# Kernel optimization log

Measured on AMD Instinct MI355X. Metric: run time of the kernel, lower is better.

## Reference

```python
import jax, jax.numpy as jnp
import numpy as np

N, E, D, EDGE_DIM = 50000, 150000, 100, 200

def _w(key, fi, fo):
    return jax.random.normal(key, (fi, fo), dtype=jnp.float32) / np.float32(np.sqrt(fi))

def setup_inputs():
    key = jax.random.key(0)
    ks = jax.random.split(key, 40)
    inp = {}
    inp["x"] = jax.random.normal(ks[0], (N, D), dtype=jnp.float32)
    inp["msg"] = jax.random.normal(ks[1], (E, D), dtype=jnp.float32)
    # TimeEncoder: Linear(1, D)
    inp["time_w"] = _w(ks[2], 1, D)
    inp["time_b"] = jnp.zeros((D,), jnp.float32)
    # TransformerConv 1: in=100, heads=8, out=100, concat -> 800
    H1 = 8 * D
    inp["c1_qw"] = _w(ks[3], D, H1); inp["c1_qb"] = jnp.zeros((H1,), jnp.float32)
    inp["c1_kw"] = _w(ks[4], D, H1); inp["c1_kb"] = jnp.zeros((H1,), jnp.float32)
    inp["c1_vw"] = _w(ks[5], D, H1); inp["c1_vb"] = jnp.zeros((H1,), jnp.float32)
    inp["c1_ew"] = _w(ks[6], EDGE_DIM, H1)  # lin_edge has no bias in PyG
    inp["c1_sw"] = _w(ks[7], D, H1); inp["c1_sb"] = jnp.zeros((H1,), jnp.float32)
    # TransformerConv 2: in=800, heads=1, out=100, concat=False
    inp["c2_qw"] = _w(ks[8], H1, D); inp["c2_qb"] = jnp.zeros((D,), jnp.float32)
    inp["c2_kw"] = _w(ks[9], H1, D); inp["c2_kb"] = jnp.zeros((D,), jnp.float32)
    inp["c2_vw"] = _w(ks[10], H1, D); inp["c2_vb"] = jnp.zeros((D,), jnp.float32)
    inp["c2_ew"] = _w(ks[11], EDGE_DIM, D)
    inp["c2_sw"] = _w(ks[12], H1, D); inp["c2_sb"] = jnp.zeros((D,), jnp.float32)
    # LinkPredictor (in_channels=100, out=2)
    inp["lp_src_w"] = _w(ks[13], D, 2 * D); inp["lp_src_b"] = jnp.zeros((2 * D,), jnp.float32)
    inp["lp_dst_w"] = _w(ks[14], D, 2 * D); inp["lp_dst_b"] = jnp.zeros((2 * D,), jnp.float32)
    inp["lp1_w"] = _w(ks[15], 4 * D, 8 * D); inp["lp1_b"] = jnp.zeros((8 * D,), jnp.float32)
    inp["lp2_w"] = _w(ks[16], 8 * D, 2 * D); inp["lp2_b"] = jnp.zeros((2 * D,), jnp.float32)
    inp["lp3_w"] = _w(ks[17], 2 * D, D // 2); inp["lp3_b"] = jnp.zeros((D // 2,), jnp.float32)
    inp["lp4_w"] = _w(ks[18], D // 2, 2); inp["lp4_b"] = jnp.zeros((2,), jnp.float32)
    inp["last_update"] = jax.random.randint(ks[19], (N,), 0, 1000000)
    inp["t"] = jax.random.randint(ks[20], (E,), 0, 1000000)
    inp["edge_index"] = jax.random.randint(ks[21], (2, E), 0, N)
    return inp

def _tconv(x, src, dst, edge_attr, qw, qb, kw, kb, vw, vb, ew, sw, sb, heads, out_ch, concat, n):
    q = (x @ qw + qb).reshape(n, heads, out_ch)
    k = (x @ kw + kb).reshape(n, heads, out_ch)
    v = (x @ vw + vb).reshape(n, heads, out_ch)
    e = (edge_attr @ ew).reshape(-1, heads, out_ch)        # [E,H,C]
    kj = k[src] + e                                        # gather src keys + edge
    alpha = jnp.sum(q[dst] * kj, axis=-1) / np.float32(np.sqrt(out_ch))  # [E,H]
    amax = jax.ops.segment_max(alpha, dst, num_segments=n)
    ex = jnp.exp(alpha - amax[dst])
    denom = jax.ops.segment_sum(ex, dst, num_segments=n)
    a = ex / (denom[dst] + 1e-16)                          # per-dest softmax
    agg = jax.ops.segment_sum((v[src] + e) * a[..., None], dst, num_segments=n)
    out = agg.reshape(n, heads * out_ch) if concat else jnp.mean(agg, axis=1)
    return out + x @ sw + sb                               # root/skip connection

def reference(x, msg, time_w, time_b,
              c1_qw, c1_qb, c1_kw, c1_kb, c1_vw, c1_vb, c1_ew, c1_sw, c1_sb,
              c2_qw, c2_qb, c2_kw, c2_kb, c2_vw, c2_vb, c2_ew, c2_sw, c2_sb,
              lp_src_w, lp_src_b, lp_dst_w, lp_dst_b,
              lp1_w, lp1_b, lp2_w, lp2_b, lp3_w, lp3_b, lp4_w, lp4_b,
              last_update, t, edge_index):
    src, dst = edge_index[0], edge_index[1]
    rel_t = (last_update[src] - t).astype(jnp.float32)[:, None]  # [E,1]
    rel_enc = jnp.cos(rel_t @ time_w + time_b)                   # [E,D]
    edge_attr = jnp.concatenate([rel_enc, msg], axis=-1)         # [E,200]
    h = jax.nn.relu(_tconv(x, src, dst, edge_attr, c1_qw, c1_qb, c1_kw, c1_kb,
                           c1_vw, c1_vb, c1_ew, c1_sw, c1_sb, 8, D, True, N))
    h = jax.nn.relu(_tconv(h, src, dst, edge_attr, c2_qw, c2_qb, c2_kw, c2_kb,
                           c2_vw, c2_vb, c2_ew, c2_sw, c2_sb, 1, D, False, N))
    hh = jnp.concatenate([h[src] @ lp_src_w + lp_src_b,
                          h[dst] @ lp_dst_w + lp_dst_b], axis=-1)
    hh = jnp.tanh(hh @ lp1_w + lp1_b)
    hh = jnp.tanh(hh @ lp2_w + lp2_b)
    hh = jnp.tanh(hh @ lp3_w + lp3_b)
    return hh @ lp4_w + lp4_b
```

## Files before the change

### kernel.cpp

```cpp
#include <hip/hip_runtime.h>
#include <hip/hip_bf16.h>
#include <math.h>

typedef __hip_bfloat16 bf16;
typedef short s16x8 __attribute__((ext_vector_type(8)));
typedef float f32x4 __attribute__((ext_vector_type(4)));

#define NN 50000
#define EE 150000
#define EH 75000

static __device__ __forceinline__ float b2f(bf16 x){ return __bfloat162float(x); }
static __device__ __forceinline__ bf16 f2b(float x){ return __float2bfloat16(x); }
static __device__ __forceinline__ short f2s(float x){
  union { bf16 b; short s; } u; u.b = f2b(x); return u.s;
}
static __device__ __forceinline__ float u2f_lo(unsigned u){ union{unsigned i;float f;}c; c.i=u<<16; return c.f; }
static __device__ __forceinline__ float u2f_hi(unsigned u){ union{unsigned i;float f;}c; c.i=u&0xffff0000u; return c.f; }

static __device__ __forceinline__ float fast_tanh(float x){
  float a = fabsf(x);
  float e = __expf(2.0f*a);
  float t = 1.0f - __fdividef(2.0f, e + 1.0f);
  return x < 0.f ? -t : t;
}

static __device__ __forceinline__ void gload_lds16(const void* g, void* l){
  __builtin_amdgcn_global_load_lds((const __attribute__((address_space(1))) void*)g,
                                   (__attribute__((address_space(3))) void*)l, 16, 0, 0);
}

__global__ void k_zero(int* __restrict__ p, int n){
  int i = blockIdx.x*blockDim.x + threadIdx.x;
  if(i<n) p[i]=0;
}

__global__ void k_hist(const int* __restrict__ dst, int* __restrict__ deg){
  int i = blockIdx.x*blockDim.x + threadIdx.x;
  if(i<EE) atomicAdd(&deg[dst[i]], 1);
}

__global__ void k_scan(const int* __restrict__ deg, int* __restrict__ rowptr){
  __shared__ int part[1024];
  int tid = threadIdx.x;
  const int n = NN;
  int chunk = (n + 1023)/1024;
  int start = tid*chunk;
  int end = start + chunk; if(end > n) end = n;
  int s = 0;
  for(int i=start;i<end;i++) s += deg[i];
  part[tid] = s; __syncthreads();
  for(int off=1; off<1024; off<<=1){
    int v = (tid>=off)? part[tid-off] : 0;
    __syncthreads();
    part[tid] += v;
    __syncthreads();
  }
  int run = (tid==0)? 0 : part[tid-1];
  for(int i=start;i<end;i++){ rowptr[i]=run; run += deg[i]; }
  if(tid==0) rowptr[n] = part[1023];
}

__global__ void k_scatter(const int* __restrict__ dst, const int* __restrict__ rowptr,
                          int* __restrict__ cursor, int* __restrict__ elist){
  int e = blockIdx.x*blockDim.x + threadIdx.x;
  if(e<EE){ int d=dst[e]; int p=atomicAdd(&cursor[d],1); elist[rowptr[d]+p]=e; }
}

__global__ void k_relenc(const int* __restrict__ src, const int* __restrict__ tt,
                         const int* __restrict__ lu, const float* __restrict__ tw,
                         const float* __restrict__ tb, bf16* __restrict__ rel){
  int i = blockIdx.x*blockDim.x + threadIdx.x;
  if(i >= EE*112) return;
  int e = i/112, c = i - e*112;
  float v = 0.f;
  if(c < 100){
    float rt  = (float)(lu[src[e]] - tt[e]);
    float arg = __fadd_rn(__fmul_rn(rt, tw[c]), tb[c]);
    v = cosf(arg);
  }
  rel[i] = f2b(v);
}

__global__ void k_cvtpad(const float* __restrict__ in, int incols,
                         bf16* __restrict__ outp, int outcols, int total){
  int i = blockIdx.x*blockDim.x + threadIdx.x;
  if(i >= total) return;
  int r = i/outcols, c = i - r*outcols;
  outp[i] = f2b(c < incols ? in[(size_t)r*incols + c] : 0.f);
}

__global__ void k_wt2(const float* __restrict__ W, int K, int N, int colofs, int ncols,
                      bf16* __restrict__ WT, int kpad, int nrows){
  int i = blockIdx.x*blockDim.x + threadIdx.x;
  if(i >= nrows*kpad) return;
  int n = i / kpad, k = i - n*kpad;
  float v = (n<ncols && k<K)? W[(size_t)k*N + colofs + n] : 0.f;
  WT[i] = f2b(v);
}

__global__ void k_wtc1(const float* __restrict__ qw, const float* __restrict__ kw,
                       const float* __restrict__ vw, const float* __restrict__ sw,
                       bf16* __restrict__ outp){
  int i = blockIdx.x*blockDim.x + threadIdx.x;
  if(i >= 8*448*128) return;
  int h = i/(448*128), r = (i/128)%448, k = i&127;
  float v = 0.f;
  if(r < 400 && k < 100){
    int s = r/100, n = r - s*100;
    const float* W = s==0? qw : s==1? kw : s==2? vw : sw;
    v = W[(size_t)k*800 + h*100 + n];
  }
  outp[i] = f2b(v);
}

__global__ void k_wte(const float* __restrict__ ew, int N, int colofs,
                      bf16* __restrict__ outp){
  int i = blockIdx.x*blockDim.x + threadIdx.x;
  if(i >= 112*256) return;
  int r = i>>8, k = i&255;
  float v = 0.f;
  if(r < 100){
    if(k < 100) v = ew[(size_t)k*N + colofs + r];
    else if(k >= 128 && k < 228) v = ew[(size_t)(k-28)*N + colofs + r];
  }
  outp[i] = f2b(v);
}

__global__ void k_bstack(const float* __restrict__ b0, const float* __restrict__ b1,
                         const float* __restrict__ b2, const float* __restrict__ b3,
                         int W, int H, float* __restrict__ outp){
  int i = blockIdx.x*blockDim.x + threadIdx.x;
  if(i >= H*4*W) return;
  int h = i/(4*W), r = i - h*4*W, s = r/W, c = r - s*W;
  const float* b = s==0? b0 : s==1? b1 : s==2? b2 : b3;
  outp[i] = b[h*W + c];
}

template<int NT>
__global__ __launch_bounds__(256) void mm_tile(
    const bf16* __restrict__ A1, int lda1, int ksplit, int k1valid,
    const float* __restrict__ A2f, int lda2, int k2valid,
    const int* __restrict__ gather,
    const bf16* __restrict__ WT, int kpad,
    const bf16* __restrict__ zbuf,
    const float* __restrict__ bias,
    bf16* __restrict__ C, int ldc,
    int M, int nvalid, int act)
{
  constexpr int BN = NT*16;
  constexpr int BP = (BN*4 + 255)/256;
  constexpr int ABYTES = 128*32*2;
  constexpr int BBYTES = BN*32*2;
  constexpr int BUFSZ  = ABYTES + BBYTES;
  __shared__ __align__(16) char lds[2*BUFSZ];

  const int tid  = threadIdx.x;
  const int wave = tid>>6, lane = tid&63;
  const int quad = lane>>4, lo = lane&15;
  const int nstrip = blockIdx.y;
  WT += (size_t)nstrip*BN*kpad;
  C  += (size_t)nstrip*BN;
  if(bias) bias += nstrip*BN;
  const int nval = nvalid - nstrip*BN;
  const int row0 = blockIdx.x*128;

  const char*  a1base[2];
  const float* a2base[2];
  int acol0[2];
#pragma unroll
  for(int p=0;p<2;p++){
    int s = p*256 + tid;
    int row = s>>2, cp = s&3;
    int q = cp ^ ((row>>1)&3);
    int col0 = q*8;
    int rg = row0 + row; if(rg > M-1) rg = M-1;
    int ar = gather ? gather[rg] : rg;
    acol0[p]  = col0;
    a1base[p] = (const char*)A1 + ((size_t)ar*lda1 + col0)*2;
    a2base[p] = A2f ? (A2f + (size_t)ar*lda2 + col0 - ksplit) : nullptr;
  }
  const char* bbase[BP];
  bool bval[BP];
#pragma unroll
  for(int q=0;q<BP;q++){
    int s = q*256 + tid;
    int rb = s>>2, cp = s&3;
    int rbc = rb < BN ? rb : BN-1;
    int lq = cp ^ ((rbc>>1)&3);
    bval[q]  = (s < BN*4);
    bbase[q] = (const char*)WT + ((size_t)rbc*kpad + lq*8)*2;
  }

  f32x4 acc[2][NT];
#pragma unroll
  for(int m=0;m<2;m++)
#pragma unroll
    for(int n=0;n<NT;n++) acc[m][n] = (f32x4){0.f,0.f,0.f,0.f};

  float4 pf0[2], pf1[2];

  auto stageA1 = [&](char* buf, int kb){
#pragma unroll
    for(int p=0;p<2;p++){
      const char* s = (kb + acol0[p] < k1valid) ? (a1base[p] + (size_t)kb*2)
                                                : (const char*)zbuf;
      gload_lds16(s, buf + p*4096 + wave*1024);
    }
  };
  auto loadA2 = [&](int kb){
#pragma unroll
    for(int p=0;p<2;p++){
      int kk = kb - ksplit + acol0[p];
      const float* ap = a2base[p] + kb;
      pf0[p] = (kk   < k2valid) ? *(const float4*)ap     : (float4){0.f,0.f,0.f,0.f};
      pf1[p] = (kk+4 < k2valid) ? *(const float4*)(ap+4) : (float4){0.f,0.f,0.f,0.f};
    }
  };
  auto writeA2 = [&](char* buf){
#pragma unroll
    for(int p=0;p<2;p++){
      s16x8 v;
      v[0]=f2s(pf0[p].x); v[1]=f2s(pf0[p].y); v[2]=f2s(pf0[p].z); v[3]=f2s(pf0[p].w);
      v[4]=f2s(pf1[p].x); v[5]=f2s(pf1[p].y); v[6]=f2s(pf1[p].z); v[7]=f2s(pf1[p].w);
      *(s16x8*)(buf + p*4096 + (size_t)tid*16) = v;
    }
  };
  auto stageB = [&](char* buf, int kb){
#pragma unroll
    for(int q=0;q<BP;q++){
      if(bval[q]) gload_lds16(bbase[q] + (size_t)kb*2, buf + ABYTES + q*4096 + wave*1024);
    }
  };
  auto compute = [&](const char* buf){
    s16x8 af[2];
#pragma unroll
    for(int m=0;m<2;m++){
      int rl = wave*32 + m*16 + lo;
      int cp = quad ^ ((rl>>1)&3);
      af[m] = *(const s16x8*)(buf + rl*64 + cp*16);
    }
#pragma unroll
    for(int n=0;n<NT;n++){
      int rb = n*16 + lo;
      int cp = quad ^ ((rb>>1)&3);
      s16x8 bfr = *(const s16x8*)(buf + ABYTES + rb*64 + cp*16);
      acc[0][n] = __builtin_amdgcn_mfma_f32_16x16x32_bf16(af[0], bfr, acc[0][n], 0,0,0);
      acc[1][n] = __builtin_amdgcn_mfma_f32_16x16x32_bf16(af[1], bfr, acc[1][n], 0,0,0);
    }
  };

  {
    char* b0 = lds;
    if(0 < ksplit || !A2f) stageA1(b0, 0);
    else { loadA2(0); writeA2(b0); }
    stageB(b0, 0);
    __syncthreads();
  }
  const int ktiles = kpad >> 5;
  for(int kt=0; kt<ktiles; kt++){
    char* cur = lds + (kt&1)*BUFSZ;
    char* nxt = lds + ((kt&1)^1)*BUFSZ;
    int nb = (kt+1)<<5;
    bool havenext = nb < kpad;
    bool fpnx = havenext && nb >= ksplit && A2f;
    if(havenext){
      if(nb < ksplit || !A2f) stageA1(nxt, nb);
      else                    loadA2(nb);
      stageB(nxt, nb);
    }
    compute(cur);
    if(fpnx) writeA2(nxt);
    __syncthreads();
  }

  const int r0 = (lane&1)<<1;
#pragma unroll
  for(int n=0;n<NT;n++){
    int col  = n*16 + lo;
    int pcol = col & ~1;
    bool cok = (pcol < nval);
    float bv = 0.f;
    if(bias && col < nval) bv = bias[col];
#pragma unroll
    for(int m=0;m<2;m++){
      float v[4];
#pragma unroll
      for(int r=0;r<4;r++){
        float t = acc[m][n][r] + bv;
        if(act==1) t = fmaxf(t, 0.f);
        else if(act==2) t = fast_tanh(t);
        v[r] = t;
      }
      unsigned mylo = (unsigned)(unsigned short)f2s(v[r0])
                    | ((unsigned)(unsigned short)f2s(v[r0+1])<<16);
      unsigned snd  = (unsigned)(unsigned short)f2s(v[r0^2])
                    | ((unsigned)(unsigned short)f2s(v[(r0^2)+1])<<16);
      unsigned got  = (unsigned)__shfl_xor((int)snd, 1);
      unsigned w0, w1;
      if(lane&1){ w0 = (got & 0xffffu) | (mylo<<16); w1 = (got>>16) | (mylo & 0xffff0000u); }
      else      { w0 = (mylo & 0xffffu) | (got<<16); w1 = (mylo>>16) | (got & 0xffff0000u); }
      if(cok){
        int prow = row0 + wave*32 + m*16 + quad*4 + r0;
        if(prow   < M) *(unsigned*)(C + (size_t)prow*ldc + pcol) = w0;
        if(prow+1 < M) *(unsigned*)(C + (size_t)(prow+1)*ldc + pcol) = w1;
      }
    }
  }
}

__global__ __launch_bounds__(256) void k_attn(
    const int* __restrict__ rowptr, const int* __restrict__ elist,
    const int* __restrict__ srcv,
    const bf16* __restrict__ qkvs, const bf16* __restrict__ eh,
    bf16* __restrict__ hout, int ldh, int colofs, int zpad)
{
  int wave = threadIdx.x>>6, lane = threadIdx.x&63;
  int node = blockIdx.x*4 + wave;
  if(node >= NN) return;
  bool act = (lane < 50);
  float q0=0.f, q1=0.f;
  const unsigned* qrow = (const unsigned*)(qkvs + (size_t)node*400);
  if(act){ unsigned u = qrow[lane]; q0=u2f_lo(u); q1=u2f_hi(u); }
  int s0 = rowptr[node], s1 = rowptr[node+1];
  float m = -3.4e38f, d = 0.f, a0 = 0.f, a1 = 0.f;
  for(int j=s0; j<s1; j++){
    int e = elist[j];
    int sn = srcv[e];
    float p = 0.f, e0=0.f, e1=0.f;
    if(act){
      unsigned uk = ((const unsigned*)(qkvs + (size_t)sn*400 + 100))[lane];
      unsigned ue = ((const unsigned*)(eh   + (size_t)e*100))[lane];
      e0=u2f_lo(ue); e1=u2f_hi(ue);
      p = q0*(u2f_lo(uk)+e0) + q1*(u2f_hi(uk)+e1);
    }
    for(int off=32; off; off>>=1) p += __shfl_xor(p, off);
    float alpha = p * 0.1f;
    float mn = fmaxf(m, alpha);
    float sc = __expf(m - mn);
    float wv = __expf(alpha - mn);
    d = d*sc + wv;
    if(act){
      unsigned uv = ((const unsigned*)(qkvs + (size_t)sn*400 + 200))[lane];
      a0 = a0*sc + wv*(u2f_lo(uv)+e0);
      a1 = a1*sc + wv*(u2f_hi(uv)+e1);
    }
    m = mn;
  }
  if(act){
    float inv = 1.f/(d + 1e-16f);
    unsigned us = ((const unsigned*)(qkvs + (size_t)node*400 + 300))[lane];
    float h0 = fmaxf(u2f_lo(us) + a0*inv, 0.f);
    float h1 = fmaxf(u2f_hi(us) + a1*inv, 0.f);
    bf16* op = hout + (size_t)node*ldh + colofs + lane*2;
    op[0] = f2b(h0); op[1] = f2b(h1);
  } else if(zpad && lane < 56){
    bf16* op = hout + (size_t)node*ldh + colofs + lane*2;
    op[0] = f2b(0.f); op[1] = f2b(0.f);
  }
}

__global__ void k_lpout(const bf16* __restrict__ t3, const float* __restrict__ w4,
                        const float* __restrict__ b4, float* __restrict__ out,
                        int base, int n){
  int i = blockIdx.x*blockDim.x + threadIdx.x;
  if(i >= n*2) return;
  int g = i>>1, j = i&1;
  const bf16* tp = t3 + (size_t)g*50;
  float s = 0.f;
  for(int k=0;k<50;k++) s += b2f(tp[k])*w4[k*2+j];
  out[(size_t)(base+g)*2 + j] = s + b4[j];
}

extern "C" void kernel_launch(void* const* d_in, const int* in_sizes, int n_in,
                              void* d_out, int out_size, void* d_ws, size_t ws_size,
                              hipStream_t stream){
  const float* x       = (const float*)d_in[0];
  const float* msg     = (const float*)d_in[1];
  const float* time_w  = (const float*)d_in[2];
  const float* time_b  = (const float*)d_in[3];
  const float* c1_qw=(const float*)d_in[4];  const float* c1_qb=(const float*)d_in[5];
  const float* c1_kw=(const float*)d_in[6];  const float* c1_kb=(const float*)d_in[7];
  const float* c1_vw=(const float*)d_in[8];  const float* c1_vb=(const float*)d_in[9];
  const float* c1_ew=(const float*)d_in[10];
  const float* c1_sw=(const float*)d_in[11]; const float* c1_sb=(const float*)d_in[12];
  const float* c2_qw=(const float*)d_in[13]; const float* c2_qb=(const float*)d_in[14];
  const float* c2_kw=(const float*)d_in[15]; const float* c2_kb=(const float*)d_in[16];
  const float* c2_vw=(const float*)d_in[17]; const float* c2_vb=(const float*)d_in[18];
  const float* c2_ew=(const float*)d_in[19];
  const float* c2_sw=(const float*)d_in[20]; const float* c2_sb=(const float*)d_in[21];
  const float* lp_src_w=(const float*)d_in[22]; const float* lp_src_b=(const float*)d_in[23];
  const float* lp_dst_w=(const float*)d_in[24]; const float* lp_dst_b=(const float*)d_in[25];
  const float* lp1_w=(const float*)d_in[26]; const float* lp1_b=(const float*)d_in[27];
  const float* lp2_w=(const float*)d_in[28]; const float* lp2_b=(const float*)d_in[29];
  const float* lp3_w=(const float*)d_in[30]; const float* lp3_b=(const float*)d_in[31];
  const float* lp4_w=(const float*)d_in[32]; const float* lp4_b=(const float*)d_in[33];
  const int* last_update=(const int*)d_in[34];
  const int* tt =(const int*)d_in[35];
  const int* edge_index=(const int*)d_in[36];
  const int* src = edge_index;
  const int* dst = edge_index + EE;
  float* out = (float*)d_out;

  char* ws = (char*)d_ws;
  bf16*  h1    = (bf16*) (ws + 0);
  bf16*  relpad= (bf16*) (ws + 80000000);
  bf16*  eh    = (bf16*) (ws + 113600000);
  bf16*  qkvs  = (bf16*) (ws + 143600000);
  bf16*  h2p   = (bf16*) (ws + 183600000);
  bf16*  xb    = (bf16*) (ws + 183600000);
  int*   rowptr= (int*)  (ws + 194800000);
  int*   elist = (int*)  (ws + 195000064);
  int*   deg   = (int*)  (ws + 195600064);
  int*   cursor= (int*)  (ws + 195800064);
  bf16* c1all  = (bf16*)(ws + 196000064);
  bf16* c1eall = (bf16*)(ws + 196917568);
  bf16* c2all  = (bf16*)(ws + 197376320);
  bf16* c2e    = (bf16*)(ws + 198179136);
  bf16* lpswt  = (bf16*)(ws + 198236480);
  bf16* lpdwt  = (bf16*)(ws + 198293824);
  bf16* lp1t   = (bf16*)(ws + 198351168);
  bf16* lp2t   = (bf16*)(ws + 199268672);
  bf16* lp3t   = (bf16*)(ws + 199670080);
  float* c1ball= (float*)(ws + 199702848);
  float* c2ball= (float*)(ws + 199715648);
  bf16* zbuf   = (bf16*)(ws + 199717248);
  bf16* lhh = (bf16*)(ws + 0);
  bf16* lt1 = (bf16*)(ws + 60000000);
  bf16* lt2 = (bf16*)(ws + 0);
  bf16* lt3 = (bf16*)(ws + 30000000);

  k_wtc1<<<(8*448*128+255)/256,256,0,stream>>>(c1_qw,c1_kw,c1_vw,c1_sw,c1all);
  for(int h=0; h<8; h++)
    k_wte<<<(112*256+255)/256,256,0,stream>>>(c1_ew, 800, h*100, c1eall + (size_t)h*112*256);
  k_wte<<<(112*256+255)/256,256,0,stream>>>(c2_ew, 100, 0, c2e);
  k_wt2<<<(100*896+255)/256,256,0,stream>>>(c2_qw,800,100,0,100,c2all,         896,100);
  k_wt2<<<(100*896+255)/256,256,0,stream>>>(c2_kw,800,100,0,100,c2all+100*896, 896,100);
  k_wt2<<<(100*896+255)/256,256,0,stream>>>(c2_vw,800,100,0,100,c2all+200*896, 896,100);
  k_wt2<<<(100*896+255)/256,256,0,stream>>>(c2_sw,800,100,0,100,c2all+300*896, 896,100);
  k_wt2<<<(48*896+255)/256,256,0,stream>>>(c2_sw,800,100,0,0,   c2all+400*896, 896,48);
  k_wt2<<<(224*128+255)/256,256,0,stream>>>(lp_src_w,100,200,0,200,lpswt,128,224);
  k_wt2<<<(224*128+255)/256,256,0,stream>>>(lp_dst_w,100,200,0,200,lpdwt,128,224);
  k_wt2<<<(896*512+255)/256,256,0,stream>>>(lp1_w,400,800,0,800,lp1t,512,896);
  k_wt2<<<(224*896+255)/256,256,0,stream>>>(lp2_w,800,200,0,200,lp2t,896,224);
  k_wt2<<<(64*256+255)/256,256,0,stream>>>(lp3_w,200,50,0,50,lp3t,256,64);
  k_bstack<<<(3200+255)/256,256,0,stream>>>(c1_qb,c1_kb,c1_vb,c1_sb,100,8,c1ball);
  k_bstack<<<(400+255)/256,256,0,stream>>>(c2_qb,c2_kb,c2_vb,c2_sb,100,1,c2ball);
  k_zero<<<1,64,0,stream>>>((int*)zbuf, 16);
  k_cvtpad<<<(NN*112+255)/256,256,0,stream>>>(x, 100, xb, 112, NN*112);

  k_zero   <<<(NN+255)/256, 256, 0, stream>>>(deg, NN);
  k_zero   <<<(NN+255)/256, 256, 0, stream>>>(cursor, NN);
  k_hist   <<<(EE+255)/256, 256, 0, stream>>>(dst, deg);
  k_scan   <<<1, 1024, 0, stream>>>(deg, rowptr);
  k_scatter<<<(EE+255)/256, 256, 0, stream>>>(dst, rowptr, cursor, elist);

  k_relenc<<<(EE*112+255)/256, 256, 0, stream>>>(src, tt, last_update, time_w, time_b, relpad);

  int gN = (NN + 127)/128;
  int gE = (EE + 127)/128;
  int gL = (EH + 127)/128;
  int gA = (NN + 3)/4;

  for(int h=0; h<8; h++){
    mm_tile<13><<<dim3(gN,2),256,0,stream>>>(xb,112,128,112, nullptr,0,0, nullptr,
        c1all + (size_t)h*448*128, 128, zbuf, c1ball + h*400, qkvs,400, NN,400,0);
    mm_tile<7><<<dim3(gE,1),256,0,stream>>>(relpad,112,128,112, msg,100,100, nullptr,
        c1eall + (size_t)h*112*256, 256, zbuf, nullptr, eh,100, EE,100,0);
    k_attn<<<gA,256,0,stream>>>(rowptr, elist, src, qkvs, eh, h1, 800, h*100, 0);
  }

  mm_tile<13><<<dim3(gN,2),256,0,stream>>>(h1,800,896,800, nullptr,0,0, nullptr,
      c2all,896, zbuf, c2ball, qkvs,400, NN,400,0);
  mm_tile<7><<<dim3(gE,1),256,0,stream>>>(relpad,112,128,112, msg,100,100, nullptr,
      c2e,256, zbuf, nullptr, eh,100, EE,100,0);
  k_attn<<<gA,256,0,stream>>>(rowptr, elist, src, qkvs, eh, h2p, 112, 0, 1);

  for(int half=0; half<2; half++){
    const int* esrc = src + half*EH;
    const int* edst = dst + half*EH;
    mm_tile<13><<<dim3(gL,1),256,0,stream>>>(h2p,112,128,112, nullptr,0,0, esrc,
        lpswt,128, zbuf, lp_src_b, lhh,400, EH,200,0);
    mm_tile<13><<<dim3(gL,1),256,0,stream>>>(h2p,112,128,112, nullptr,0,0, edst,
        lpdwt,128, zbuf, lp_dst_b, lhh+200,400, EH,200,0);
    mm_tile<10><<<dim3(gL,5),256,0,stream>>>(lhh,400,512,400, nullptr,0,0, nullptr,
        lp1t,512, zbuf, lp1_b, lt1,800, EH,800,2);
    mm_tile<13><<<dim3(gL,1),256,0,stream>>>(lt1,800,896,800, nullptr,0,0, nullptr,
        lp2t,896, zbuf, lp2_b, lt2,200, EH,200,2);
    mm_tile<4><<<dim3(gL,1),256,0,stream>>>(lt2,200,256,200, nullptr,0,0, nullptr,
        lp3t,256, zbuf, lp3_b, lt3,50, EH,50,2);
    k_lpout<<<(EH*2+255)/256,256,0,stream>>>(lt3, lp4_w, lp4_b, out, half*EH, EH);
  }

  (void)in_sizes; (void)n_in; (void)out_size; (void)ws_size;
}
```

Measured before the change: 2.281 ms.

## Fold link-predictor linears, triple-buffer GEMM pipeline, retune tiles and padding

```diff
diff --git a/kernel.cpp b/kernel.cpp
--- a/kernel.cpp
+++ b/kernel.cpp
@@ -28,6 +28,22 @@
 static __device__ __forceinline__ void gload_lds16(const void* g, void* l){
   __builtin_amdgcn_global_load_lds((const __attribute__((address_space(1))) void*)g,
                                    (__attribute__((address_space(3))) void*)l, 16, 0, 0);
+}
+
+template<int N> static __device__ __forceinline__ void wait_vmcnt(){
+  if constexpr(N==0) asm volatile("s_waitcnt vmcnt(0)" ::: "memory");
+  else if constexpr(N==1) asm volatile("s_waitcnt vmcnt(1)" ::: "memory");
+  else if constexpr(N==2) asm volatile("s_waitcnt vmcnt(2)" ::: "memory");
+  else if constexpr(N==3) asm volatile("s_waitcnt vmcnt(3)" ::: "memory");
+  else if constexpr(N==4) asm volatile("s_waitcnt vmcnt(4)" ::: "memory");
+  else if constexpr(N==5) asm volatile("s_waitcnt vmcnt(5)" ::: "memory");
+  else asm volatile("s_waitcnt vmcnt(6)" ::: "memory");
+}
+static __device__ __forceinline__ void wait_lgkm0(){
+  asm volatile("s_waitcnt lgkmcnt(0)" ::: "memory");
+}
+static __device__ __forceinline__ void memfence(){
+  asm volatile("" ::: "memory");
 }
 
 __global__ void k_zero(int* __restrict__ p, int n){
@@ -137,11 +153,36 @@
   outp[i] = b[h*W + c];
 }
 
+__global__ void k_foldw(const float* __restrict__ sw, const float* __restrict__ dw,
+                        const float* __restrict__ w1, bf16* __restrict__ o){
+  int i = blockIdx.x*blockDim.x + threadIdx.x;
+  if(i >= 800*224) return;
+  int n = i/224, k = i - n*224;
+  float s = 0.f;
+  if(k < 100){
+    for(int j=0;j<200;j++) s += sw[k*200+j]*w1[(size_t)j*800+n];
+  } else if(k >= 112 && k < 212){
+    int kk = k-112;
+    for(int j=0;j<200;j++) s += dw[kk*200+j]*w1[(size_t)(200+j)*800+n];
+  }
+  o[i] = f2b(s);
+}
+__global__ void k_foldb(const float* __restrict__ sb, const float* __restrict__ db,
+                        const float* __restrict__ w1, const float* __restrict__ b1,
+                        float* __restrict__ o){
+  int n = blockIdx.x*blockDim.x + threadIdx.x;
+  if(n >= 800) return;
+  float s = b1[n];
+  for(int j=0;j<200;j++) s += sb[j]*w1[(size_t)j*800+n] + db[j]*w1[(size_t)(200+j)*800+n];
+  o[n] = s;
+}
+
 template<int NT>
 __global__ __launch_bounds__(256) void mm_tile(
-    const bf16* __restrict__ A1, int lda1, int ksplit, int k1valid,
-    const float* __restrict__ A2f, int lda2, int k2valid,
-    const int* __restrict__ gather,
+    const bf16* __restrict__ A1, int lda1, int kv1, const int* __restrict__ g1,
+    int KS,
+    const bf16* __restrict__ A2b, int lda2b, int kv2b, const int* __restrict__ g2,
+    const float* __restrict__ A2f, int lda2f, int kv2f,
     const bf16* __restrict__ WT, int kpad,
     const bf16* __restrict__ zbuf,
     const float* __restrict__ bias,
@@ -149,11 +190,10 @@
     int M, int nvalid, int act)
 {
   constexpr int BN = NT*16;
-  constexpr int BP = (BN*4 + 255)/256;
-  constexpr int ABYTES = 128*32*2;
-  constexpr int BBYTES = BN*32*2;
-  constexpr int BUFSZ  = ABYTES + BBYTES;
-  __shared__ __align__(16) char lds[2*BUFSZ];
+  constexpr int BPASS = (BN*4 + 255)/256;
+  constexpr int ABYTES = 8192;
+  constexpr int BUFSZ = ABYTES + BPASS*4096;
+  __shared__ __align__(16) char lds[3*BUFSZ];
 
   const int tid  = threadIdx.x;
   const int wave = tid>>6, lane = tid&63;
@@ -165,8 +205,18 @@
   const int nval = nvalid - nstrip*BN;
   const int row0 = blockIdx.x*128;
 
-  const char*  a1base[2];
-  const float* a2base[2];
+  float bvr[NT];
+#pragma unroll
+  for(int n=0;n<NT;n++){
+    int col = n*16 + lo;
+    bvr[n] = (bias && col < nval) ? bias[col] : 0.f;
+  }
+#pragma unroll
+  for(int n=0;n<NT;n++) asm volatile("" :: "v"(bvr[n]));
+
+  const char*  a1b[2];
+  const char*  a2b[2];
+  const float* f2base[2];
   int acol0[2];
 #pragma unroll
   for(int p=0;p<2;p++){
@@ -175,21 +225,21 @@
     int q = cp ^ ((row>>1)&3);
     int col0 = q*8;
     int rg = row0 + row; if(rg > M-1) rg = M-1;
-    int ar = gather ? gather[rg] : rg;
-    acol0[p]  = col0;
-    a1base[p] = (const char*)A1 + ((size_t)ar*lda1 + col0)*2;
-    a2base[p] = A2f ? (A2f + (size_t)ar*lda2 + col0 - ksplit) : nullptr;
-  }
-  const char* bbase[BP];
-  bool bval[BP];
-#pragma unroll
-  for(int q=0;q<BP;q++){
-    int s = q*256 + tid;
-    int rb = s>>2, cp = s&3;
-    int rbc = rb < BN ? rb : BN-1;
-    int lq = cp ^ ((rbc>>1)&3);
-    bval[q]  = (s < BN*4);
-    bbase[q] = (const char*)WT + ((size_t)rbc*kpad + lq*8)*2;
+    int r1 = g1 ? g1[rg] : rg;
+    int r2 = g2 ? g2[rg] : rg;
+    acol0[p] = col0;
+    a1b[p]   = (const char*)A1 + ((size_t)r1*lda1 + col0)*2;
+    a2b[p]   = A2b ? (const char*)A2b + ((size_t)r2*lda2b)*2 : nullptr;
+    f2base[p]= A2f ? (A2f + (size_t)rg*lda2f) : nullptr;
+  }
+  const char* bbase[BPASS];
+#pragma unroll
+  for(int p=0;p<BPASS;p++){
+    int s = p*256 + tid;
+    int rb = s>>2; if(rb > BN-1) rb = BN-1;
+    int cp = s&3;
+    int lq = cp ^ ((rb>>1)&3);
+    bbase[p] = (const char*)WT + ((size_t)rb*kpad + lq*8)*2;
   }
 
   f32x4 acc[2][NT];
@@ -203,18 +253,20 @@
   auto stageA1 = [&](char* buf, int kb){
 #pragma unroll
     for(int p=0;p<2;p++){
-      const char* s = (kb + acol0[p] < k1valid) ? (a1base[p] + (size_t)kb*2)
-                                                : (const char*)zbuf;
+      int k = kb + acol0[p];
+      const char* s;
+      if(k < KS) s = (k < kv1) ? (a1b[p] + (size_t)kb*2) : (const char*)zbuf;
+      else { int o = k - KS; s = (o < kv2b) ? (a2b[p] + (size_t)o*2) : (const char*)zbuf; }
       gload_lds16(s, buf + p*4096 + wave*1024);
     }
   };
-  auto loadA2 = [&](int kb){
+  auto loadA2f = [&](int kb){
 #pragma unroll
     for(int p=0;p<2;p++){
-      int kk = kb - ksplit + acol0[p];
-      const float* ap = a2base[p] + kb;
-      pf0[p] = (kk   < k2valid) ? *(const float4*)ap     : (float4){0.f,0.f,0.f,0.f};
-      pf1[p] = (kk+4 < k2valid) ? *(const float4*)(ap+4) : (float4){0.f,0.f,0.f,0.f};
+      int o = kb + acol0[p] - KS;
+      const float* ap = f2base[p] + o;
+      pf0[p] = (o   < kv2f) ? *(const float4*)ap     : (float4){0.f,0.f,0.f,0.f};
+      pf1[p] = (o+4 < kv2f) ? *(const float4*)(ap+4) : (float4){0.f,0.f,0.f,0.f};
     }
   };
   auto writeA2 = [&](char* buf){
@@ -228,9 +280,8 @@
   };
   auto stageB = [&](char* buf, int kb){
 #pragma unroll
-    for(int q=0;q<BP;q++){
-      if(bval[q]) gload_lds16(bbase[q] + (size_t)kb*2, buf + ABYTES + q*4096 + wave*1024);
-    }
+    for(int p=0;p<BPASS;p++)
+      gload_lds16(bbase[p] + (size_t)kb*2, buf + ABYTES + p*4096 + wave*1024);
   };
   auto compute = [&](const char* buf){
     s16x8 af[2];
@@ -250,28 +301,31 @@
     }
   };
 
-  {
-    char* b0 = lds;
-    if(0 < ksplit || !A2f) stageA1(b0, 0);
-    else { loadA2(0); writeA2(b0); }
-    stageB(b0, 0);
-    __syncthreads();
-  }
-  const int ktiles = kpad >> 5;
-  for(int kt=0; kt<ktiles; kt++){
-    char* cur = lds + (kt&1)*BUFSZ;
-    char* nxt = lds + ((kt&1)^1)*BUFSZ;
-    int nb = (kt+1)<<5;
-    bool havenext = nb < kpad;
-    bool fpnx = havenext && nb >= ksplit && A2f;
-    if(havenext){
-      if(nb < ksplit || !A2f) stageA1(nxt, nb);
-      else                    loadA2(nb);
-      stageB(nxt, nb);
-    }
-    compute(cur);
-    if(fpnx) writeA2(nxt);
-    __syncthreads();
+  const int T = kpad >> 5;
+  stageA1(lds, 0); stageB(lds, 0);
+  if(T > 1){ stageA1(lds + BUFSZ, 32); stageB(lds + BUFSZ, 32); }
+
+  for(int t=0; t<T; t++){
+    bool nb  = (t+1 < T);
+    bool nfp = nb && A2f && (((t+1)<<5) >= KS);
+    if(!nb)      wait_vmcnt<0>();
+    else if(nfp) wait_vmcnt<BPASS>();
+    else         wait_vmcnt<2+BPASS>();
+    wait_lgkm0();
+    __builtin_amdgcn_s_barrier();
+    memfence();
+    int tp = t+2;
+    bool sp  = (tp < T);
+    bool spf = sp && A2f && ((tp<<5) >= KS);
+    char* nb3 = lds + (tp%3)*BUFSZ;
+    if(sp){
+      int kb2 = tp<<5;
+      if(spf) loadA2f(kb2);
+      else    stageA1(nb3, kb2);
+      stageB(nb3, kb2);
+    }
+    compute(lds + (t%3)*BUFSZ);
+    if(spf) writeA2(nb3);
   }
 
   const int r0 = (lane&1)<<1;
@@ -280,8 +334,7 @@
     int col  = n*16 + lo;
     int pcol = col & ~1;
     bool cok = (pcol < nval);
-    float bv = 0.f;
-    if(bias && col < nval) bv = bias[col];
+    float bv = bvr[n];
 #pragma unroll
     for(int m=0;m<2;m++){
       float v[4];
@@ -417,33 +470,30 @@
   bf16* c1eall = (bf16*)(ws + 196917568);
   bf16* c2all  = (bf16*)(ws + 197376320);
   bf16* c2e    = (bf16*)(ws + 198179136);
-  bf16* lpswt  = (bf16*)(ws + 198236480);
-  bf16* lpdwt  = (bf16*)(ws + 198293824);
-  bf16* lp1t   = (bf16*)(ws + 198351168);
+  bf16* lp1tF  = (bf16*)(ws + 198351168);
   bf16* lp2t   = (bf16*)(ws + 199268672);
   bf16* lp3t   = (bf16*)(ws + 199670080);
   float* c1ball= (float*)(ws + 199702848);
   float* c2ball= (float*)(ws + 199715648);
   bf16* zbuf   = (bf16*)(ws + 199717248);
-  bf16* lhh = (bf16*)(ws + 0);
-  bf16* lt1 = (bf16*)(ws + 60000000);
-  bf16* lt2 = (bf16*)(ws + 0);
-  bf16* lt3 = (bf16*)(ws + 30000000);
+  float* lp1c  = (float*)(ws + 199717312);
+  bf16* lt1 = (bf16*)(ws + 0);
+  bf16* lt2 = (bf16*)(ws + 120000000);
+  bf16* lt3 = (bf16*)(ws + 150000000);
 
   k_wtc1<<<(8*448*128+255)/256,256,0,stream>>>(c1_qw,c1_kw,c1_vw,c1_sw,c1all);
   for(int h=0; h<8; h++)
     k_wte<<<(112*256+255)/256,256,0,stream>>>(c1_ew, 800, h*100, c1eall + (size_t)h*112*256);
   k_wte<<<(112*256+255)/256,256,0,stream>>>(c2_ew, 100, 0, c2e);
-  k_wt2<<<(100*896+255)/256,256,0,stream>>>(c2_qw,800,100,0,100,c2all,         896,100);
-  k_wt2<<<(100*896+255)/256,256,0,stream>>>(c2_kw,800,100,0,100,c2all+100*896, 896,100);
-  k_wt2<<<(100*896+255)/256,256,0,stream>>>(c2_vw,800,100,0,100,c2all+200*896, 896,100);
-  k_wt2<<<(100*896+255)/256,256,0,stream>>>(c2_sw,800,100,0,100,c2all+300*896, 896,100);
-  k_wt2<<<(48*896+255)/256,256,0,stream>>>(c2_sw,800,100,0,0,   c2all+400*896, 896,48);
-  k_wt2<<<(224*128+255)/256,256,0,stream>>>(lp_src_w,100,200,0,200,lpswt,128,224);
-  k_wt2<<<(224*128+255)/256,256,0,stream>>>(lp_dst_w,100,200,0,200,lpdwt,128,224);
-  k_wt2<<<(896*512+255)/256,256,0,stream>>>(lp1_w,400,800,0,800,lp1t,512,896);
-  k_wt2<<<(224*896+255)/256,256,0,stream>>>(lp2_w,800,200,0,200,lp2t,896,224);
-  k_wt2<<<(64*256+255)/256,256,0,stream>>>(lp3_w,200,50,0,50,lp3t,256,64);
+  k_wt2<<<(100*800+255)/256,256,0,stream>>>(c2_qw,800,100,0,100,c2all,         800,100);
+  k_wt2<<<(100*800+255)/256,256,0,stream>>>(c2_kw,800,100,0,100,c2all+100*800, 800,100);
+  k_wt2<<<(100*800+255)/256,256,0,stream>>>(c2_vw,800,100,0,100,c2all+200*800, 800,100);
+  k_wt2<<<(100*800+255)/256,256,0,stream>>>(c2_sw,800,100,0,100,c2all+300*800, 800,100);
+  k_wt2<<<(48*800+255)/256,256,0,stream>>>(c2_sw,800,100,0,0,   c2all+400*800, 800,48);
+  k_wt2<<<(224*800+255)/256,256,0,stream>>>(lp2_w,800,200,0,200,lp2t,800,224);
+  k_wt2<<<(64*224+255)/256,256,0,stream>>>(lp3_w,200,50,0,50,lp3t,224,64);
+  k_foldw<<<(800*224+255)/256,256,0,stream>>>(lp_src_w, lp_dst_w, lp1_w, lp1tF);
+  k_foldb<<<(800+255)/256,256,0,stream>>>(lp_src_b, lp_dst_b, lp1_w, lp1_b, lp1c);
   k_bstack<<<(3200+255)/256,256,0,stream>>>(c1_qb,c1_kb,c1_vb,c1_sb,100,8,c1ball);
   k_bstack<<<(400+255)/256,256,0,stream>>>(c2_qb,c2_kb,c2_vb,c2_sb,100,1,c2ball);
   k_zero<<<1,64,0,stream>>>((int*)zbuf, 16);
@@ -463,32 +513,35 @@
   int gA = (NN + 3)/4;
 
   for(int h=0; h<8; h++){
-    mm_tile<13><<<dim3(gN,2),256,0,stream>>>(xb,112,128,112, nullptr,0,0, nullptr,
+    mm_tile<9><<<dim3(gN,3),256,0,stream>>>(xb,112,112,nullptr, 128,
+        nullptr,0,0,nullptr, nullptr,0,0,
         c1all + (size_t)h*448*128, 128, zbuf, c1ball + h*400, qkvs,400, NN,400,0);
-    mm_tile<7><<<dim3(gE,1),256,0,stream>>>(relpad,112,128,112, msg,100,100, nullptr,
+    mm_tile<7><<<dim3(gE,1),256,0,stream>>>(relpad,112,112,nullptr, 128,
+        nullptr,0,0,nullptr, msg,100,100,
         c1eall + (size_t)h*112*256, 256, zbuf, nullptr, eh,100, EE,100,0);
     k_attn<<<gA,256,0,stream>>>(rowptr, elist, src, qkvs, eh, h1, 800, h*100, 0);
   }
 
-  mm_tile<13><<<dim3(gN,2),256,0,stream>>>(h1,800,896,800, nullptr,0,0, nullptr,
-      c2all,896, zbuf, c2ball, qkvs,400, NN,400,0);
-  mm_tile<7><<<dim3(gE,1),256,0,stream>>>(relpad,112,128,112, msg,100,100, nullptr,
+  mm_tile<9><<<dim3(gN,3),256,0,stream>>>(h1,800,800,nullptr, 800,
+      nullptr,0,0,nullptr, nullptr,0,0,
+      c2all,800, zbuf, c2ball, qkvs,400, NN,400,0);
+  mm_tile<7><<<dim3(gE,1),256,0,stream>>>(relpad,112,112,nullptr, 128,
+      nullptr,0,0,nullptr, msg,100,100,
       c2e,256, zbuf, nullptr, eh,100, EE,100,0);
   k_attn<<<gA,256,0,stream>>>(rowptr, elist, src, qkvs, eh, h2p, 112, 0, 1);
 
   for(int half=0; half<2; half++){
     const int* esrc = src + half*EH;
     const int* edst = dst + half*EH;
-    mm_tile<13><<<dim3(gL,1),256,0,stream>>>(h2p,112,128,112, nullptr,0,0, esrc,
-        lpswt,128, zbuf, lp_src_b, lhh,400, EH,200,0);
-    mm_tile<13><<<dim3(gL,1),256,0,stream>>>(h2p,112,128,112, nullptr,0,0, edst,
-        lpdwt,128, zbuf, lp_dst_b, lhh+200,400, EH,200,0);
-    mm_tile<10><<<dim3(gL,5),256,0,stream>>>(lhh,400,512,400, nullptr,0,0, nullptr,
-        lp1t,512, zbuf, lp1_b, lt1,800, EH,800,2);
-    mm_tile<13><<<dim3(gL,1),256,0,stream>>>(lt1,800,896,800, nullptr,0,0, nullptr,
-        lp2t,896, zbuf, lp2_b, lt2,200, EH,200,2);
-    mm_tile<4><<<dim3(gL,1),256,0,stream>>>(lt2,200,256,200, nullptr,0,0, nullptr,
-        lp3t,256, zbuf, lp3_b, lt3,50, EH,50,2);
+    mm_tile<10><<<dim3(gL,5),256,0,stream>>>(h2p,112,112,esrc, 112,
+        h2p,112,112,edst, nullptr,0,0,
+        lp1tF,224, zbuf, lp1c, lt1,800, EH,800,2);
+    mm_tile<7><<<dim3(gL,2),256,0,stream>>>(lt1,800,800,nullptr, 800,
+        nullptr,0,0,nullptr, nullptr,0,0,
+        lp2t,800, zbuf, lp2_b, lt2,200, EH,200,2);
+    mm_tile<4><<<dim3(gL,1),256,0,stream>>>(lt2,200,200,nullptr, 224,
+        nullptr,0,0,nullptr, nullptr,0,0,
+        lp3t,224, zbuf, lp3_b, lt3,50, EH,50,2);
     k_lpout<<<(EH*2+255)/256,256,0,stream>>>(lt3, lp4_w, lp4_b, out, half*EH, EH);
   }
 
```

Measured after the change: 2.025 ms. 11.2% less time.
